# Optimization experiments

Hardware: AMD Instinct MI355X
Metric: run time of the kernel (lower is better)

The kernel has to match this reference:

```python
import jax, jax.numpy as jnp
import numpy as np

N_NODES = 50000
N_EDGES = 800000
IN_C, HID_C, OUT_C = 64, 64, 32


def setup_inputs() -> dict:
    key = jax.random.key(0)
    ks = jax.random.split(key, 8)
    x = jax.random.normal(ks[0], (N_NODES, IN_C), dtype=jnp.float32)
    edge_index = jax.random.randint(ks[1], (2, N_EDGES), 0, N_NODES, dtype=jnp.int64)
    s1 = 1.0 / np.sqrt(IN_C)
    s2 = 1.0 / np.sqrt(HID_C)
    W_rel1 = jax.random.uniform(ks[2], (IN_C, HID_C), jnp.float32, -s1, s1)
    W_root1 = jax.random.uniform(ks[3], (IN_C, HID_C), jnp.float32, -s1, s1)
    b1 = jax.random.uniform(ks[4], (HID_C,), jnp.float32, -s1, s1)
    W_rel2 = jax.random.uniform(ks[5], (HID_C, OUT_C), jnp.float32, -s2, s2)
    W_root2 = jax.random.uniform(ks[6], (HID_C, OUT_C), jnp.float32, -s2, s2)
    b2 = jax.random.uniform(ks[7], (OUT_C,), jnp.float32, -s2, s2)
    return {"x": x, "edge_index": edge_index, "W_rel1": W_rel1, "W_root1": W_root1,
            "b1": b1, "W_rel2": W_rel2, "W_root2": W_root2, "b2": b2}


def _graph_conv(x, src, dst, W_rel, W_root, b):
    # aggregate neighbor features (sum over incoming edges), then linear
    agg = jax.ops.segment_sum(x[src], dst, num_segments=N_NODES)  # [N, C_in]
    return agg @ W_rel + x @ W_root + b


def reference(x, edge_index, W_rel1, W_root1, b1, W_rel2, W_root2, b2):
    src, dst = edge_index[0], edge_index[1]
    h = jax.nn.relu(_graph_conv(x, src, dst, W_rel1, W_root1, b1))
    out = _graph_conv(h, src, dst, W_rel2, W_root2, b2)
    return out
```

## Files before the change

kernel.cpp:

```cpp
#include <hip/hip_runtime.h>

static constexpr int N_NODES = 50000;
static constexpr int N_EDGES = 800000;

static constexpr int NBK      = 196;
static constexpr int BCAP     = 5120;
static constexpr int MAXE     = BCAP / 512;
static constexpr int BIN_TILE = 2048;
static constexpr int BIN_BLOCKS = (N_EDGES + BIN_TILE - 1) / BIN_TILE;
static constexpr int PRE1_TILES  = (N_NODES + 15) / 16;
static constexpr int PRE1_BLOCKS = (PRE1_TILES + 3) / 4;

typedef __attribute__((ext_vector_type(8))) short   bf16x8;
typedef __attribute__((ext_vector_type(4))) float   floatx4;

__device__ __forceinline__ unsigned short f2b(float f) {
    union { float f; unsigned u; } v; v.f = f;
    unsigned r = v.u + 0x7FFFu + ((v.u >> 16) & 1u);
    return (unsigned short)(r >> 16);
}
__device__ __forceinline__ float blo(unsigned v) {
    union { unsigned u; float f; } c; c.u = v << 16; return c.f;
}
__device__ __forceinline__ float bhi(unsigned v) {
    union { unsigned u; float f; } c; c.u = v & 0xffff0000u; return c.f;
}
__device__ __forceinline__ unsigned pk2(float a, float b) {
    return (unsigned)f2b(a) | ((unsigned)f2b(b) << 16);
}

__device__ __forceinline__ void bin_body(
    int bb, const int* __restrict__ srcv, const int* __restrict__ dstv,
    int* __restrict__ bcnt, unsigned* __restrict__ epair)
{
    __shared__ uint2 stage[BIN_TILE];
    __shared__ int cnt[256];
    __shared__ int scn[256];
    __shared__ int pref[NBK];
    __shared__ int gbase[NBK];

    int tid   = threadIdx.x;
    int base  = bb * BIN_TILE;
    int tileN = min(BIN_TILE, N_EDGES - base);

    cnt[tid] = 0;
    __syncthreads();

    int ss[8], dd[8], sl[8];
#pragma unroll
    for (int j = 0; j < 8; ++j) {
        int i = tid + j * 256;
        ss[j] = -1; dd[j] = 0; sl[j] = 0;
        if (i < tileN) {
            ss[j] = srcv[base + i];
            dd[j] = dstv[base + i];
            sl[j] = atomicAdd(&cnt[dd[j] >> 8], 1);
        }
    }
    __syncthreads();

    int own = cnt[tid];
    scn[tid] = own;
    __syncthreads();
    for (int off = 1; off < 256; off <<= 1) {
        int t = (tid >= off) ? scn[tid - off] : 0;
        __syncthreads();
        scn[tid] += t;
        __syncthreads();
    }
    if (tid < NBK) {
        pref[tid]  = scn[tid] - cnt[tid];
        gbase[tid] = tid * BCAP + atomicAdd(&bcnt[tid], cnt[tid]);
    }
    __syncthreads();

#pragma unroll
    for (int j = 0; j < 8; ++j) {
        if (ss[j] >= 0) {
            int b = dd[j] >> 8;
            stage[pref[b] + sl[j]] = uint2{(unsigned)ss[j], (unsigned)dd[j]};
        }
    }
    __syncthreads();

    for (int i = tid; i < tileN; i += 256) {
        uint2 pd = stage[i];
        int b = (int)(pd.y >> 8);
        epair[(size_t)gbase[b] + (i - pref[b])] = (pd.x << 8) | (pd.y & 255u);
    }
}

__device__ __forceinline__ void pre1_body(
    int bb, const float* __restrict__ x,
    const float* __restrict__ Wrel, const float* __restrict__ Wroot,
    const float* __restrict__ bias,
    unsigned short* __restrict__ u1, unsigned short* __restrict__ r1)
{
    int lane = threadIdx.x & 63;
    int c15  = lane & 15;
    int q    = lane >> 4;

    bf16x8 bf[2][4][2];
#pragma unroll
    for (int mat = 0; mat < 2; ++mat) {
        const float* W = mat ? Wroot : Wrel;
#pragma unroll
        for (int ct = 0; ct < 4; ++ct) {
            int c = ct * 16 + c15;
#pragma unroll
            for (int kf = 0; kf < 2; ++kf) {
                int kb = kf * 32 + q * 8;
                bf16x8 f;
#pragma unroll
                for (int j = 0; j < 8; ++j)
                    f[j] = (short)f2b(W[(kb + j) * 64 + c]);
                bf[mat][ct][kf] = f;
            }
        }
    }
    float bv[4];
#pragma unroll
    for (int ct = 0; ct < 4; ++ct) bv[ct] = bias[ct * 16 + c15];

    int tile = bb * 4 + (threadIdx.x >> 6);
    if (tile * 16 >= N_NODES) return;
    int row0 = tile * 16;

    const float* xr = x + (size_t)(row0 + c15) * 64;
    bf16x8 a0, a1;
#pragma unroll
    for (int j = 0; j < 8; ++j) {
        a0[j] = (short)f2b(xr[q * 8 + j]);
        a1[j] = (short)f2b(xr[32 + q * 8 + j]);
    }

    floatx4 z = {0.f, 0.f, 0.f, 0.f};
    floatx4 acc[2][4];
#pragma unroll
    for (int mat = 0; mat < 2; ++mat)
#pragma unroll
        for (int ct = 0; ct < 4; ++ct) {
            floatx4 a = __builtin_amdgcn_mfma_f32_16x16x32_bf16(a0, bf[mat][ct][0], z, 0, 0, 0);
            acc[mat][ct] = __builtin_amdgcn_mfma_f32_16x16x32_bf16(a1, bf[mat][ct][1], a, 0, 0, 0);
        }

#pragma unroll
    for (int reg = 0; reg < 4; ++reg) {
        int row = row0 + q * 4 + reg;
        uint2 uu, rr;
        uu.x = pk2(acc[0][0][reg],          acc[0][1][reg]);
        uu.y = pk2(acc[0][2][reg],          acc[0][3][reg]);
        rr.x = pk2(acc[1][0][reg] + bv[0],  acc[1][1][reg] + bv[1]);
        rr.y = pk2(acc[1][2][reg] + bv[2],  acc[1][3][reg] + bv[3]);
        *reinterpret_cast<uint2*>(u1 + (size_t)row * 64 + c15 * 4) = uu;
        *reinterpret_cast<uint2*>(r1 + (size_t)row * 64 + c15 * 4) = rr;
    }
}

__global__ __launch_bounds__(256) void k_binpre1(
    const int* __restrict__ srcv, const int* __restrict__ dstv,
    int* __restrict__ bcnt, unsigned* __restrict__ epair,
    const float* __restrict__ x,
    const float* __restrict__ Wrel, const float* __restrict__ Wroot,
    const float* __restrict__ bias,
    unsigned short* __restrict__ u1, unsigned short* __restrict__ r1)
{
    if ((int)blockIdx.x < BIN_BLOCKS)
        bin_body(blockIdx.x, srcv, dstv, bcnt, epair);
    else
        pre1_body(blockIdx.x - BIN_BLOCKS, x, Wrel, Wroot, bias, u1, r1);
}

__global__ __launch_bounds__(512) void k_build(
    const unsigned* __restrict__ epair, const int* __restrict__ bcnt,
    int* __restrict__ offsets, int* __restrict__ esrc)
{
    __shared__ int cnt[256];
    __shared__ int scn[256];
    __shared__ int start[256];
    __shared__ int s_base;

    int b = blockIdx.x;
    int t = threadIdx.x;
    int node0 = b << 8;
    int ncnt  = min(256, N_NODES - node0);
    int beg   = b * BCAP;
    int m     = bcnt[b];

    if (t < 256) cnt[t] = 0;
    __syncthreads();

    unsigned ev[MAXE]; int sl[MAXE];
#pragma unroll
    for (int j = 0; j < MAXE; ++j) {
        int i = t + j * 512;
        ev[j] = 0; sl[j] = -1;
        if (i < m) {
            ev[j] = epair[beg + i];
            sl[j] = atomicAdd(&cnt[ev[j] & 255u], 1);
        }
    }

    if (t < 64) {
        int pre = 0;
#pragma unroll
        for (int k = 0; k < 4; ++k) {
            int i = t + (k << 6);
            if (i < b) pre += bcnt[i];
        }
        for (int off = 1; off < 64; off <<= 1) pre += __shfl_xor(pre, off);
        if (t == 0) s_base = pre;
    }
    __syncthreads();

    int own = (t < 256) ? cnt[t] : 0;
    if (t < 256) scn[t] = own;
    __syncthreads();
    for (int off = 1; off < 256; off <<= 1) {
        int v = (t < 256 && t >= off) ? scn[t - off] : 0;
        __syncthreads();
        if (t < 256) scn[t] += v;
        __syncthreads();
    }
    if (t < 256) {
        int st = s_base + scn[t] - own;
        start[t] = st;
        if (t < ncnt) offsets[node0 + t] = st;
    }
    if (b == 0 && t == 0) offsets[N_NODES] = N_EDGES;
    __syncthreads();

#pragma unroll
    for (int j = 0; j < MAXE; ++j) {
        if (sl[j] >= 0)
            esrc[start[ev[j] & 255u] + sl[j]] = (int)(ev[j] >> 8);
    }
}

__global__ __launch_bounds__(256) void k_aggp2(
    const unsigned short* __restrict__ u1,
    const unsigned short* __restrict__ r1,
    const int* __restrict__ offsets, const int* __restrict__ esrc,
    const float* __restrict__ Wrel,
    const float* __restrict__ Wroot,
    const float* __restrict__ bias,
    unsigned short* __restrict__ u2,
    unsigned short* __restrict__ r2)
{
    __shared__ unsigned short hlds[64 * 64];

    int w    = threadIdx.x >> 6;
    int lane = threadIdx.x & 63;
    int j    = lane & 7;
    int slot = lane >> 3;

    for (int t = 0; t < 16; ++t) {
        int nl   = w * 16 + t;
        int node = blockIdx.x * 64 + nl;
        if (node < N_NODES) {
            int beg = offsets[node], end = offsets[node + 1];
            float s0 = 0.f, s1 = 0.f, s2 = 0.f, s3 = 0.f;
            float s4 = 0.f, s5 = 0.f, s6 = 0.f, s7 = 0.f;
            for (int e = beg + slot; e < end; e += 8) {
                int sv = esrc[e];
                uint4 v = *reinterpret_cast<const uint4*>(u1 + (size_t)sv * 64 + j * 8);
                s0 += blo(v.x); s1 += bhi(v.x);
                s2 += blo(v.y); s3 += bhi(v.y);
                s4 += blo(v.z); s5 += bhi(v.z);
                s6 += blo(v.w); s7 += bhi(v.w);
            }
            s0 += __shfl_xor(s0, 32); s1 += __shfl_xor(s1, 32);
            s2 += __shfl_xor(s2, 32); s3 += __shfl_xor(s3, 32);
            s4 += __shfl_xor(s4, 32); s5 += __shfl_xor(s5, 32);
            s6 += __shfl_xor(s6, 32); s7 += __shfl_xor(s7, 32);
            s0 += __shfl_xor(s0, 16); s1 += __shfl_xor(s1, 16);
            s2 += __shfl_xor(s2, 16); s3 += __shfl_xor(s3, 16);
            s4 += __shfl_xor(s4, 16); s5 += __shfl_xor(s5, 16);
            s6 += __shfl_xor(s6, 16); s7 += __shfl_xor(s7, 16);
            s0 += __shfl_xor(s0, 8);  s1 += __shfl_xor(s1, 8);
            s2 += __shfl_xor(s2, 8);  s3 += __shfl_xor(s3, 8);
            s4 += __shfl_xor(s4, 8);  s5 += __shfl_xor(s5, 8);
            s6 += __shfl_xor(s6, 8);  s7 += __shfl_xor(s7, 8);
            if (lane < 8) {
                uint4 rv = *reinterpret_cast<const uint4*>(r1 + (size_t)node * 64 + j * 8);
                float v0 = fmaxf(s0 + blo(rv.x), 0.f);
                float v1 = fmaxf(s1 + bhi(rv.x), 0.f);
                float v2 = fmaxf(s2 + blo(rv.y), 0.f);
                float v3 = fmaxf(s3 + bhi(rv.y), 0.f);
                float v4 = fmaxf(s4 + blo(rv.z), 0.f);
                float v5 = fmaxf(s5 + bhi(rv.z), 0.f);
                float v6 = fmaxf(s6 + blo(rv.w), 0.f);
                float v7 = fmaxf(s7 + bhi(rv.w), 0.f);
                uint4 o;
                o.x = pk2(v0, v1); o.y = pk2(v2, v3);
                o.z = pk2(v4, v5); o.w = pk2(v6, v7);
                unsigned byte = (unsigned)nl * 128u + (((unsigned)j * 16u) ^ (((unsigned)nl & 7u) << 4));
                *reinterpret_cast<uint4*>((char*)hlds + byte) = o;
            }
        }
    }
    __syncthreads();

    int c15 = lane & 15;
    int q   = lane >> 4;
    int row0l = w * 16;
    int row0  = blockIdx.x * 64 + row0l;
    if (row0 >= N_NODES) return;

    bf16x8 bf[2][2][2];
#pragma unroll
    for (int mat = 0; mat < 2; ++mat) {
        const float* W = mat ? Wroot : Wrel;
#pragma unroll
        for (int ct = 0; ct < 2; ++ct) {
            int c = ct * 16 + c15;
#pragma unroll
            for (int kf = 0; kf < 2; ++kf) {
                bf16x8 f;
#pragma unroll
                for (int jj = 0; jj < 8; ++jj) {
                    int p = kf * 32 + q * 8 + jj;
                    int tk = (p & 3) * 16 + (p >> 2);
                    f[jj] = (short)f2b(W[tk * 32 + c]);
                }
                bf[mat][ct][kf] = f;
            }
        }
    }
    float bv[2];
#pragma unroll
    for (int ct = 0; ct < 2; ++ct) bv[ct] = bias[ct * 16 + c15];

    int r = row0l + c15;
    unsigned sw = ((unsigned)r & 7u) << 4;
    bf16x8 a0 = *reinterpret_cast<const bf16x8*>((char*)hlds + (unsigned)r * 128u + (((unsigned)q * 16u) ^ sw));
    bf16x8 a1 = *reinterpret_cast<const bf16x8*>((char*)hlds + (unsigned)r * 128u + ((((unsigned)q + 4u) * 16u) ^ sw));

    floatx4 z = {0.f, 0.f, 0.f, 0.f};
    floatx4 acc[2][2];
#pragma unroll
    for (int mat = 0; mat < 2; ++mat)
#pragma unroll
        for (int ct = 0; ct < 2; ++ct) {
            floatx4 a = __builtin_amdgcn_mfma_f32_16x16x32_bf16(a0, bf[mat][ct][0], z, 0, 0, 0);
            acc[mat][ct] = __builtin_amdgcn_mfma_f32_16x16x32_bf16(a1, bf[mat][ct][1], a, 0, 0, 0);
        }

#pragma unroll
    for (int reg = 0; reg < 4; ++reg) {
        int row = row0 + q * 4 + reg;
        unsigned uu = pk2(acc[0][0][reg],         acc[0][1][reg]);
        unsigned rr = pk2(acc[1][0][reg] + bv[0], acc[1][1][reg] + bv[1]);
        *reinterpret_cast<unsigned*>(u2 + (size_t)row * 32 + c15 * 2) = uu;
        *reinterpret_cast<unsigned*>(r2 + (size_t)row * 32 + c15 * 2) = rr;
    }
}

__global__ __launch_bounds__(256) void k_agg32(
    const unsigned short* __restrict__ u2,
    const unsigned short* __restrict__ r2,
    const int* __restrict__ offsets, const int* __restrict__ esrc,
    float* __restrict__ out)
{
    int lane = threadIdx.x & 63;
    int node = (blockIdx.x * blockDim.x + threadIdx.x) >> 6;
    if (node >= N_NODES) return;
    int j    = lane & 3;
    int slot = lane >> 2;
    int beg = offsets[node], end = offsets[node + 1];
    float s0 = 0.f, s1 = 0.f, s2 = 0.f, s3 = 0.f;
    float s4 = 0.f, s5 = 0.f, s6 = 0.f, s7 = 0.f;
    for (int e = beg + slot; e < end; e += 16) {
        int sv = esrc[e];
        uint4 v = *reinterpret_cast<const uint4*>(u2 + (size_t)sv * 32 + j * 8);
        s0 += blo(v.x); s1 += bhi(v.x);
        s2 += blo(v.y); s3 += bhi(v.y);
        s4 += blo(v.z); s5 += bhi(v.z);
        s6 += blo(v.w); s7 += bhi(v.w);
    }
    s0 += __shfl_xor(s0, 32); s1 += __shfl_xor(s1, 32);
    s2 += __shfl_xor(s2, 32); s3 += __shfl_xor(s3, 32);
    s4 += __shfl_xor(s4, 32); s5 += __shfl_xor(s5, 32);
    s6 += __shfl_xor(s6, 32); s7 += __shfl_xor(s7, 32);
    s0 += __shfl_xor(s0, 16); s1 += __shfl_xor(s1, 16);
    s2 += __shfl_xor(s2, 16); s3 += __shfl_xor(s3, 16);
    s4 += __shfl_xor(s4, 16); s5 += __shfl_xor(s5, 16);
    s6 += __shfl_xor(s6, 16); s7 += __shfl_xor(s7, 16);
    s0 += __shfl_xor(s0, 8);  s1 += __shfl_xor(s1, 8);
    s2 += __shfl_xor(s2, 8);  s3 += __shfl_xor(s3, 8);
    s4 += __shfl_xor(s4, 8);  s5 += __shfl_xor(s5, 8);
    s6 += __shfl_xor(s6, 8);  s7 += __shfl_xor(s7, 8);
    s0 += __shfl_xor(s0, 4);  s1 += __shfl_xor(s1, 4);
    s2 += __shfl_xor(s2, 4);  s3 += __shfl_xor(s3, 4);
    s4 += __shfl_xor(s4, 4);  s5 += __shfl_xor(s5, 4);
    s6 += __shfl_xor(s6, 4);  s7 += __shfl_xor(s7, 4);
    if (lane < 4) {
        uint4 rv = *reinterpret_cast<const uint4*>(r2 + (size_t)node * 32 + j * 8);
        float4 oA, oB;
        oA.x = s0 + blo(rv.x);  oB.x = s1 + bhi(rv.x);
        oA.y = s2 + blo(rv.y);  oB.y = s3 + bhi(rv.y);
        oA.z = s4 + blo(rv.z);  oB.z = s5 + bhi(rv.z);
        oA.w = s6 + blo(rv.w);  oB.w = s7 + bhi(rv.w);
        *reinterpret_cast<float4*>(out + (size_t)node * 32 + j * 4)      = oA;
        *reinterpret_cast<float4*>(out + (size_t)node * 32 + 16 + j * 4) = oB;
    }
}

extern "C" void kernel_launch(void* const* d_in, const int* in_sizes, int n_in,
                              void* d_out, int out_size, void* d_ws, size_t ws_size,
                              hipStream_t stream) {
    const float* x      = (const float*)d_in[0];
    const int*   ei     = (const int*)  d_in[1];
    const float* Wrel1  = (const float*)d_in[2];
    const float* Wroot1 = (const float*)d_in[3];
    const float* b1     = (const float*)d_in[4];
    const float* Wrel2  = (const float*)d_in[5];
    const float* Wroot2 = (const float*)d_in[6];
    const float* b2     = (const float*)d_in[7];
    float*       out    = (float*)d_out;

    const int* srcv = ei;
    const int* dstv = ei + N_EDGES;

    char* p = (char*)d_ws;
    auto alloc = [&](size_t bytes) {
        char* r = p;
        p += (bytes + 255) & ~(size_t)255;
        return r;
    };
    int*      offsets = (int*)     alloc(sizeof(int) * (N_NODES + 1));
    int*      bcnt    = (int*)     alloc(sizeof(int) * NBK);
    unsigned* epair   = (unsigned*)alloc(sizeof(unsigned) * (size_t)NBK * BCAP);
    int*      esrc    = (int*)     alloc(sizeof(int) * N_EDGES);
    unsigned short* u1 = (unsigned short*)alloc(sizeof(short) * (size_t)N_NODES * 64);
    unsigned short* r1 = (unsigned short*)alloc(sizeof(short) * (size_t)N_NODES * 64);
    unsigned short* u2 = (unsigned short*)alloc(sizeof(short) * (size_t)N_NODES * 32);
    unsigned short* r2 = (unsigned short*)alloc(sizeof(short) * (size_t)N_NODES * 32);

    const int nodeBlocks = (N_NODES * 64 + 255) / 256;
    const int aggBlocks  = (N_NODES + 63) / 64;

    hipMemsetAsync(bcnt, 0, sizeof(int) * NBK, stream);
    k_binpre1<<<BIN_BLOCKS + PRE1_BLOCKS, 256, 0, stream>>>(
        srcv, dstv, bcnt, epair, x, Wrel1, Wroot1, b1, u1, r1);
    k_build<<<NBK, 512, 0, stream>>>(epair, bcnt, offsets, esrc);

    k_aggp2<<<aggBlocks, 256, 0, stream>>>(u1, r1, offsets, esrc,
                                           Wrel2, Wroot2, b2, u2, r2);

    k_agg32<<<nodeBlocks, 256, 0, stream>>>(u2, r2, offsets, esrc, out);
}
```

Before: 103.2 us.

## Restructure layer-2 aggregation to one node per wave in 1024-thread blocks

The fused aggregate-plus-transform kernel now assigns one node to each of 16 waves per 1024-thread block, instead of having 4 waves each loop serially over 16 nodes. After the barrier, only two waves run the MFMA step: one computes the Wrel product and the other the Wroot product plus bias. This gives more independent gather work in flight and shortens the per-wave serial chain. In exchange, every block reloads and converts the weights for only 16 rows, and 14 of the 16 waves sit idle during the matrix multiply.

```diff
diff --git a/kernel.cpp b/kernel.cpp
--- a/kernel.cpp
+++ b/kernel.cpp
@@ -237,7 +237,7 @@
     }
 }
 
-__global__ __launch_bounds__(256) void k_aggp2(
+__global__ __launch_bounds__(1024) void k_aggf(
     const unsigned short* __restrict__ u1,
     const unsigned short* __restrict__ r1,
     const int* __restrict__ offsets, const int* __restrict__ esrc,
@@ -247,112 +247,103 @@
     unsigned short* __restrict__ u2,
     unsigned short* __restrict__ r2)
 {
-    __shared__ unsigned short hlds[64 * 64];
+    __shared__ unsigned short hlds[16 * 64];
 
     int w    = threadIdx.x >> 6;
     int lane = threadIdx.x & 63;
     int j    = lane & 7;
     int slot = lane >> 3;
 
-    for (int t = 0; t < 16; ++t) {
-        int nl   = w * 16 + t;
-        int node = blockIdx.x * 64 + nl;
-        if (node < N_NODES) {
-            int beg = offsets[node], end = offsets[node + 1];
-            float s0 = 0.f, s1 = 0.f, s2 = 0.f, s3 = 0.f;
-            float s4 = 0.f, s5 = 0.f, s6 = 0.f, s7 = 0.f;
-            for (int e = beg + slot; e < end; e += 8) {
-                int sv = esrc[e];
-                uint4 v = *reinterpret_cast<const uint4*>(u1 + (size_t)sv * 64 + j * 8);
-                s0 += blo(v.x); s1 += bhi(v.x);
-                s2 += blo(v.y); s3 += bhi(v.y);
-                s4 += blo(v.z); s5 += bhi(v.z);
-                s6 += blo(v.w); s7 += bhi(v.w);
-            }
-            s0 += __shfl_xor(s0, 32); s1 += __shfl_xor(s1, 32);
-            s2 += __shfl_xor(s2, 32); s3 += __shfl_xor(s3, 32);
-            s4 += __shfl_xor(s4, 32); s5 += __shfl_xor(s5, 32);
-            s6 += __shfl_xor(s6, 32); s7 += __shfl_xor(s7, 32);
-            s0 += __shfl_xor(s0, 16); s1 += __shfl_xor(s1, 16);
-            s2 += __shfl_xor(s2, 16); s3 += __shfl_xor(s3, 16);
-            s4 += __shfl_xor(s4, 16); s5 += __shfl_xor(s5, 16);
-            s6 += __shfl_xor(s6, 16); s7 += __shfl_xor(s7, 16);
-            s0 += __shfl_xor(s0, 8);  s1 += __shfl_xor(s1, 8);
-            s2 += __shfl_xor(s2, 8);  s3 += __shfl_xor(s3, 8);
-            s4 += __shfl_xor(s4, 8);  s5 += __shfl_xor(s5, 8);
-            s6 += __shfl_xor(s6, 8);  s7 += __shfl_xor(s7, 8);
-            if (lane < 8) {
-                uint4 rv = *reinterpret_cast<const uint4*>(r1 + (size_t)node * 64 + j * 8);
-                float v0 = fmaxf(s0 + blo(rv.x), 0.f);
-                float v1 = fmaxf(s1 + bhi(rv.x), 0.f);
-                float v2 = fmaxf(s2 + blo(rv.y), 0.f);
-                float v3 = fmaxf(s3 + bhi(rv.y), 0.f);
-                float v4 = fmaxf(s4 + blo(rv.z), 0.f);
-                float v5 = fmaxf(s5 + bhi(rv.z), 0.f);
-                float v6 = fmaxf(s6 + blo(rv.w), 0.f);
-                float v7 = fmaxf(s7 + bhi(rv.w), 0.f);
-                uint4 o;
-                o.x = pk2(v0, v1); o.y = pk2(v2, v3);
-                o.z = pk2(v4, v5); o.w = pk2(v6, v7);
-                unsigned byte = (unsigned)nl * 128u + (((unsigned)j * 16u) ^ (((unsigned)nl & 7u) << 4));
-                *reinterpret_cast<uint4*>((char*)hlds + byte) = o;
-            }
-        }
-    }
-    __syncthreads();
-
+    int node = blockIdx.x * 16 + w;
+    if (node < N_NODES) {
+        int beg = offsets[node], end = offsets[node + 1];
+        float s0 = 0.f, s1 = 0.f, s2 = 0.f, s3 = 0.f;
+        float s4 = 0.f, s5 = 0.f, s6 = 0.f, s7 = 0.f;
+        for (int e = beg + slot; e < end; e += 8) {
+            int sv = esrc[e];
+            uint4 v = *reinterpret_cast<const uint4*>(u1 + (size_t)sv * 64 + j * 8);
+            s0 += blo(v.x); s1 += bhi(v.x);
+            s2 += blo(v.y); s3 += bhi(v.y);
+            s4 += blo(v.z); s5 += bhi(v.z);
+            s6 += blo(v.w); s7 += bhi(v.w);
+        }
+        s0 += __shfl_xor(s0, 32); s1 += __shfl_xor(s1, 32);
+        s2 += __shfl_xor(s2, 32); s3 += __shfl_xor(s3, 32);
+        s4 += __shfl_xor(s4, 32); s5 += __shfl_xor(s5, 32);
+        s6 += __shfl_xor(s6, 32); s7 += __shfl_xor(s7, 32);
+        s0 += __shfl_xor(s0, 16); s1 += __shfl_xor(s1, 16);
+        s2 += __shfl_xor(s2, 16); s3 += __shfl_xor(s3, 16);
+        s4 += __shfl_xor(s4, 16); s5 += __shfl_xor(s5, 16);
+        s6 += __shfl_xor(s6, 16); s7 += __shfl_xor(s7, 16);
+        s0 += __shfl_xor(s0, 8);  s1 += __shfl_xor(s1, 8);
+        s2 += __shfl_xor(s2, 8);  s3 += __shfl_xor(s3, 8);
+        s4 += __shfl_xor(s4, 8);  s5 += __shfl_xor(s5, 8);
+        s6 += __shfl_xor(s6, 8);  s7 += __shfl_xor(s7, 8);
+        if (lane < 8) {
+            uint4 rv = *reinterpret_cast<const uint4*>(r1 + (size_t)node * 64 + j * 8);
+            float v0 = fmaxf(s0 + blo(rv.x), 0.f);
+            float v1 = fmaxf(s1 + bhi(rv.x), 0.f);
+            float v2 = fmaxf(s2 + blo(rv.y), 0.f);
+            float v3 = fmaxf(s3 + bhi(rv.y), 0.f);
+            float v4 = fmaxf(s4 + blo(rv.z), 0.f);
+            float v5 = fmaxf(s5 + bhi(rv.z), 0.f);
+            float v6 = fmaxf(s6 + blo(rv.w), 0.f);
+            float v7 = fmaxf(s7 + bhi(rv.w), 0.f);
+            uint4 o;
+            o.x = pk2(v0, v1); o.y = pk2(v2, v3);
+            o.z = pk2(v4, v5); o.w = pk2(v6, v7);
+            unsigned byte = (unsigned)w * 128u + (((unsigned)j * 16u) ^ (((unsigned)w & 7u) << 4));
+            *reinterpret_cast<uint4*>((char*)hlds + byte) = o;
+        }
+    }
+    __syncthreads();
+
+    if (w >= 2) return;
+    int row0 = blockIdx.x * 16;
+    if (row0 >= N_NODES) return;
     int c15 = lane & 15;
     int q   = lane >> 4;
-    int row0l = w * 16;
-    int row0  = blockIdx.x * 64 + row0l;
-    if (row0 >= N_NODES) return;
-
-    bf16x8 bf[2][2][2];
-#pragma unroll
-    for (int mat = 0; mat < 2; ++mat) {
-        const float* W = mat ? Wroot : Wrel;
-#pragma unroll
-        for (int ct = 0; ct < 2; ++ct) {
-            int c = ct * 16 + c15;
-#pragma unroll
-            for (int kf = 0; kf < 2; ++kf) {
-                bf16x8 f;
-#pragma unroll
-                for (int jj = 0; jj < 8; ++jj) {
-                    int p = kf * 32 + q * 8 + jj;
-                    int tk = (p & 3) * 16 + (p >> 2);
-                    f[jj] = (short)f2b(W[tk * 32 + c]);
-                }
-                bf[mat][ct][kf] = f;
+
+    const float* W = w ? Wroot : Wrel;
+    bf16x8 bf[2][2];
+#pragma unroll
+    for (int ct = 0; ct < 2; ++ct) {
+        int c = ct * 16 + c15;
+#pragma unroll
+        for (int kf = 0; kf < 2; ++kf) {
+            bf16x8 f;
+#pragma unroll
+            for (int jj = 0; jj < 8; ++jj) {
+                int p = kf * 32 + q * 8 + jj;
+                int tk = (p & 3) * 16 + (p >> 2);
+                f[jj] = (short)f2b(W[tk * 32 + c]);
             }
+            bf[ct][kf] = f;
         }
     }
     float bv[2];
 #pragma unroll
-    for (int ct = 0; ct < 2; ++ct) bv[ct] = bias[ct * 16 + c15];
-
-    int r = row0l + c15;
+    for (int ct = 0; ct < 2; ++ct) bv[ct] = w ? bias[ct * 16 + c15] : 0.0f;
+
+    int r = c15;
     unsigned sw = ((unsigned)r & 7u) << 4;
     bf16x8 a0 = *reinterpret_cast<const bf16x8*>((char*)hlds + (unsigned)r * 128u + (((unsigned)q * 16u) ^ sw));
     bf16x8 a1 = *reinterpret_cast<const bf16x8*>((char*)hlds + (unsigned)r * 128u + ((((unsigned)q + 4u) * 16u) ^ sw));
 
     floatx4 z = {0.f, 0.f, 0.f, 0.f};
-    floatx4 acc[2][2];
-#pragma unroll
-    for (int mat = 0; mat < 2; ++mat)
-#pragma unroll
-        for (int ct = 0; ct < 2; ++ct) {
-            floatx4 a = __builtin_amdgcn_mfma_f32_16x16x32_bf16(a0, bf[mat][ct][0], z, 0, 0, 0);
-            acc[mat][ct] = __builtin_amdgcn_mfma_f32_16x16x32_bf16(a1, bf[mat][ct][1], a, 0, 0, 0);
-        }
-
+    floatx4 acc[2];
+#pragma unroll
+    for (int ct = 0; ct < 2; ++ct) {
+        floatx4 a = __builtin_amdgcn_mfma_f32_16x16x32_bf16(a0, bf[ct][0], z, 0, 0, 0);
+        acc[ct] = __builtin_amdgcn_mfma_f32_16x16x32_bf16(a1, bf[ct][1], a, 0, 0, 0);
+    }
+
+    unsigned short* dst = w ? r2 : u2;
 #pragma unroll
     for (int reg = 0; reg < 4; ++reg) {
         int row = row0 + q * 4 + reg;
-        unsigned uu = pk2(acc[0][0][reg],         acc[0][1][reg]);
-        unsigned rr = pk2(acc[1][0][reg] + bv[0], acc[1][1][reg] + bv[1]);
-        *reinterpret_cast<unsigned*>(u2 + (size_t)row * 32 + c15 * 2) = uu;
-        *reinterpret_cast<unsigned*>(r2 + (size_t)row * 32 + c15 * 2) = rr;
+        unsigned vv = pk2(acc[0][reg] + bv[0], acc[1][reg] + bv[1]);
+        *reinterpret_cast<unsigned*>(dst + (size_t)row * 32 + c15 * 2) = vv;
     }
 }
 
@@ -438,15 +429,15 @@
     unsigned short* r2 = (unsigned short*)alloc(sizeof(short) * (size_t)N_NODES * 32);
 
     const int nodeBlocks = (N_NODES * 64 + 255) / 256;
-    const int aggBlocks  = (N_NODES + 63) / 64;
+    const int aggfBlocks = (N_NODES + 15) / 16;
 
     hipMemsetAsync(bcnt, 0, sizeof(int) * NBK, stream);
     k_binpre1<<<BIN_BLOCKS + PRE1_BLOCKS, 256, 0, stream>>>(
         srcv, dstv, bcnt, epair, x, Wrel1, Wroot1, b1, u1, r1);
     k_build<<<NBK, 512, 0, stream>>>(epair, bcnt, offsets, esrc);
 
-    k_aggp2<<<aggBlocks, 256, 0, stream>>>(u1, r1, offsets, esrc,
-                                           Wrel2, Wroot2, b2, u2, r2);
+    k_aggf<<<aggfBlocks, 1024, 0, stream>>>(u1, r1, offsets, esrc,
+                                            Wrel2, Wroot2, b2, u2, r2);
 
     k_agg32<<<nodeBlocks, 256, 0, stream>>>(u2, r2, offsets, esrc, out);
 }
```

Measured after the change: 89.64 us, median of 2. -13.1%, faster.
